# Kernel optimization log

Measured on AMD Instinct MI355X. Metric: run time of the kernel, lower is better.

## Reference

```python
import jax, jax.numpy as jnp
import numpy as np

ALPHA, BETA, GAMMA = 0.1, 0.15, 0.005
W1, W2, SHIFT = 10.0, 3.0, 0.0


def _pairwise_sq_dist(x):
    # x: [B, C, N] -> [B, N, N] of sum_c (x[..,n] - x[..,m])^2, computed cdist-style
    # to avoid materializing the [B, C, N, N] broadcasted intermediate.
    sq = jnp.sum(x * x, axis=1)                      # [B, N]
    gram = jnp.einsum('bcn,bcm->bnm', x, x)          # [B, N, N]
    d = sq[:, :, None] + sq[:, None, :] - 2.0 * gram
    return jnp.maximum(d, 0.0)


def setup_inputs() -> dict:
    key = jax.random.key(0)
    k1, k2, k3 = jax.random.split(key, 3)
    B, CG, CF, H, W, N = 8, 3, 128, 224, 224, 2048
    guidance = jax.random.normal(k1, (B, CG, H, W), dtype=jnp.float32)
    features = jax.random.normal(k2, (B, CF, H, W), dtype=jnp.float32)
    coords = jax.random.randint(k3, (2, N), 0, H)    # H == W == 224
    return {"guidance": guidance, "features": features, "coords": coords}


def reference(guidance, features, coords):
    H, W = guidance.shape[2], guidance.shape[3]
    # normalized coordinates: [2, N]
    norm_coords = coords.astype(jnp.float32) / jnp.array([[H], [W]], dtype=jnp.float32)
    # coord_diff: [1, N, N]
    coord_diff = jnp.sum(
        (norm_coords[:, :, None] - norm_coords[:, None, :]) ** 2, axis=0
    )[None]

    # gather sampled pixels: [B, C, N]
    sel_guidance = guidance[:, :, coords[0], coords[1]]
    sel_feats = features[:, :, coords[0], coords[1]]

    guidance_diff = _pairwise_sq_dist(sel_guidance)  # [B, N, N]
    feat_diff = _pairwise_sq_dist(sel_feats)         # [B, N, N]

    sim_kernel = (
        W1 * jnp.exp(-coord_diff / (2.0 * ALPHA) - guidance_diff / (2.0 * BETA))
        + W2 * jnp.exp(-coord_diff / (2.0 * GAMMA))
        - SHIFT
    )
    return jnp.mean(feat_diff * sim_kernel)
```

## Files before the change

kernel.cpp:

```cpp
#include <hip/hip_runtime.h>
#include <hip/hip_bf16.h>

#define BATCH 8
#define CGUID 3
#define CFEAT 128
#define IMH 224
#define IMW 224
#define NPTS 2048
#define HWSZ (IMH * IMW)

#define TILES 16
#define NPAIR 136
#define BM 128
#define BK 64
#define LDT 72

typedef __attribute__((ext_vector_type(8))) short bf16x8;
typedef __attribute__((ext_vector_type(4))) float f32x4;

__device__ __forceinline__ ushort f2bf(float f) {
  unsigned x = __float_as_uint(f);
  unsigned r = (x + 0x7fffu + ((x >> 16) & 1u)) >> 16;
  return (ushort)r;
}
__device__ __forceinline__ float bf2f(ushort u) {
  return __uint_as_float(((unsigned)u) << 16);
}

__global__ __launch_bounds__(256) void gather_kernel(
    const float* __restrict__ guidance, const float* __restrict__ features,
    const int* __restrict__ coords,
    ushort* __restrict__ selF, float4* __restrict__ g4, float2* __restrict__ c2)
{
  int wid  = threadIdx.x >> 6;
  int lane = threadIdx.x & 63;
  int pid  = blockIdx.x * 4 + wid;
  int b = pid >> 11;
  int n = pid & (NPTS - 1);

  int y = coords[n];
  int x = coords[NPTS + n];

  size_t fbase = ((size_t)b * CFEAT) * HWSZ + (size_t)y * IMW + x;
  float f0 = features[fbase + (size_t)lane * HWSZ];
  float f1 = features[fbase + (size_t)(lane + 64) * HWSZ];

  ushort u0 = f2bf(f0), u1 = f2bf(f1);
  size_t so = (size_t)pid * CFEAT;
  selF[so + lane]      = u0;
  selF[so + 64 + lane] = u1;

  float ff0 = bf2f(u0), ff1 = bf2f(u1);
  float s = ff0 * ff0 + ff1 * ff1;
  #pragma unroll
  for (int o = 32; o > 0; o >>= 1) s += __shfl_down(s, o);

  float gc = 0.f;
  if (lane < CGUID)
    gc = guidance[((size_t)b * CGUID + lane) * HWSZ + (size_t)y * IMW + x];
  float g0 = __shfl(gc, 0), g1 = __shfl(gc, 1), g2 = __shfl(gc, 2);

  if (lane == 0) {
    g4[pid] = make_float4(g0, g1, g2, s);
    if (b == 0)
      c2[n] = make_float2((float)y / 224.0f, (float)x / 224.0f);
  }
}

__global__ __launch_bounds__(256) void crf_kernel(
    const ushort* __restrict__ selF, const float4* __restrict__ g4,
    const float2* __restrict__ c2, float* __restrict__ out)
{
  __shared__ ushort As[BM * LDT];
  __shared__ ushort Bs[BM * LDT];
  __shared__ float4 egN[BM], egM[BM];
  __shared__ float2 ecN[BM], ecM[BM];
  __shared__ float red[4];

  int b = blockIdx.x / NPAIR;
  int p = blockIdx.x % NPAIR;
  int ti = 0, rem = p;
  while (rem >= TILES - ti) { rem -= TILES - ti; ++ti; }
  int tj = ti + rem;
  int nb0 = ti * BM, mb0 = tj * BM;

  int t = threadIdx.x;
  int lane = t & 63, wid = t >> 6;
  int wr = wid >> 1, wc = wid & 1;

  if (t < BM) {
    egN[t] = g4[b * NPTS + nb0 + t];
    ecN[t] = c2[nb0 + t];
  } else {
    int q = t - BM;
    egM[q] = g4[b * NPTS + mb0 + q];
    ecM[q] = c2[mb0 + q];
  }

  f32x4 acc[4][4];
  #pragma unroll
  for (int i = 0; i < 4; ++i)
    #pragma unroll
    for (int j = 0; j < 4; ++j) acc[i][j] = (f32x4)0.f;

  const ushort* SA = selF + ((size_t)b * NPTS + nb0) * CFEAT;
  const ushort* SB = selF + ((size_t)b * NPTS + mb0) * CFEAT;

  for (int kk = 0; kk < 2; ++kk) {
    __syncthreads();
    #pragma unroll
    for (int pass = 0; pass < 4; ++pass) {
      int idx = t + pass * 256;
      int row = idx >> 3, q = idx & 7;
      int4 va = *(const int4*)(SA + (size_t)row * CFEAT + kk * BK + q * 8);
      *(int4*)(&As[row * LDT + q * 8]) = va;
      int4 vb = *(const int4*)(SB + (size_t)row * CFEAT + kk * BK + q * 8);
      *(int4*)(&Bs[row * LDT + q * 8]) = vb;
    }
    __syncthreads();
    #pragma unroll
    for (int k2 = 0; k2 < 2; ++k2) {
      int kb = k2 * 32 + (lane >> 4) * 8;
      bf16x8 a[4], bv[4];
      #pragma unroll
      for (int i = 0; i < 4; ++i)
        a[i] = *(const bf16x8*)(&As[(wr * 64 + i * 16 + (lane & 15)) * LDT + kb]);
      #pragma unroll
      for (int j = 0; j < 4; ++j)
        bv[j] = *(const bf16x8*)(&Bs[(wc * 64 + j * 16 + (lane & 15)) * LDT + kb]);
      #pragma unroll
      for (int i = 0; i < 4; ++i)
        #pragma unroll
        for (int j = 0; j < 4; ++j)
          acc[i][j] = __builtin_amdgcn_mfma_f32_16x16x32_bf16(a[i], bv[j], acc[i][j], 0, 0, 0);
    }
  }

  float sum = 0.f;
  int mlo = lane & 15, nhi = lane >> 4;
  #pragma unroll
  for (int i = 0; i < 4; ++i) {
    #pragma unroll
    for (int r = 0; r < 4; ++r) {
      int n = wr * 64 + i * 16 + nhi * 4 + r;
      float4 gn = egN[n];
      float2 cn = ecN[n];
      #pragma unroll
      for (int j = 0; j < 4; ++j) {
        int m = wc * 64 + j * 16 + mlo;
        float4 gm = egM[m];
        float2 cm = ecM[m];
        float df = gn.w + gm.w - 2.0f * acc[i][j][r];
        df = fmaxf(df, 0.0f);
        float d0 = gn.x - gm.x, d1 = gn.y - gm.y, d2 = gn.z - gm.z;
        float dg = d0 * d0 + d1 * d1 + d2 * d2;
        float dy = cn.x - cm.x, dx = cn.y - cm.y;
        float dc = dy * dy + dx * dx;
        float sim = 10.0f * __expf(-5.0f * dc - 3.3333333f * dg)
                  +  3.0f * __expf(-100.0f * dc);
        sum += df * sim;
      }
    }
  }

  #pragma unroll
  for (int o = 32; o > 0; o >>= 1) sum += __shfl_down(sum, o);
  if (lane == 0) red[wid] = sum;
  __syncthreads();
  if (t == 0) {
    float tot = red[0] + red[1] + red[2] + red[3];
    float factor = (ti == tj ? 1.0f : 2.0f) * (1.0f / (8.0f * 2048.0f * 2048.0f));
    atomicAdd(out, tot * factor);
  }
}

extern "C" void kernel_launch(void* const* d_in, const int* in_sizes, int n_in,
                              void* d_out, int out_size, void* d_ws, size_t ws_size,
                              hipStream_t stream) {
  const float* guidance = (const float*)d_in[0];
  const float* features = (const float*)d_in[1];
  const int*   coords   = (const int*)d_in[2];
  float* out = (float*)d_out;

  char* ws = (char*)d_ws;
  ushort* selF = (ushort*)ws;
  float4* g4   = (float4*)(ws + (size_t)BATCH * NPTS * CFEAT * 2);
  float2* c2   = (float2*)(ws + (size_t)BATCH * NPTS * CFEAT * 2
                              + (size_t)BATCH * NPTS * 16);

  hipMemsetAsync(d_out, 0, sizeof(float), stream);
  gather_kernel<<<BATCH * NPTS / 4, 256, 0, stream>>>(guidance, features, coords,
                                                      selF, g4, c2);
  crf_kernel<<<BATCH * NPAIR, 256, 0, stream>>>(selF, g4, c2, out);
}
```

Before: 303.2 us.

## Sort sample points by row and gather features channel-major with transpose pass

Adds a single-block counting sort of the sample coordinates by row, so neighbouring threads gather from nearby pixels and share cache lines. The gather is restructured so each thread handles one point across 16 channels, with coalesced channel-major stores, atomic accumulation of squared norms, and a separate transpose kernel that produces the point-major bf16 layout the MFMA kernel expects. The memset is folded into the sort kernel. This adds two extra launches, a serial prefix scan in one block, and an extra round trip through the workspace.

```diff
diff --git a/kernel.cpp b/kernel.cpp
--- a/kernel.cpp
+++ b/kernel.cpp
@@ -27,54 +27,104 @@
   return __uint_as_float(((unsigned)u) << 16);
 }
 
+__global__ __launch_bounds__(256) void sort_kernel(
+    const int* __restrict__ coords,
+    int* __restrict__ slin, float2* __restrict__ sc2,
+    float* __restrict__ sq, float* __restrict__ out)
+{
+  __shared__ int ys[NPTS], xs[NPTS];
+  __shared__ int hist[IMH], offs[IMH];
+  int t = threadIdx.x;
+  for (int i = t; i < IMH; i += 256) hist[i] = 0;
+  __syncthreads();
+  for (int i = t; i < NPTS; i += 256) {
+    int y = coords[i], x = coords[NPTS + i];
+    ys[i] = y; xs[i] = x;
+    atomicAdd(&hist[y], 1);
+  }
+  __syncthreads();
+  if (t == 0) {
+    int run = 0;
+    for (int i = 0; i < IMH; ++i) { offs[i] = run; run += hist[i]; }
+  }
+  __syncthreads();
+  for (int i = t; i < NPTS; i += 256) {
+    int y = ys[i], x = xs[i];
+    int r = atomicAdd(&offs[y], 1);
+    slin[r] = y * IMW + x;
+    sc2[r] = make_float2((float)y / 224.0f, (float)x / 224.0f);
+  }
+  for (int i = t; i < BATCH * NPTS; i += 256) sq[i] = 0.0f;
+  if (t == 0) out[0] = 0.0f;
+}
+
 __global__ __launch_bounds__(256) void gather_kernel(
-    const float* __restrict__ guidance, const float* __restrict__ features,
-    const int* __restrict__ coords,
-    ushort* __restrict__ selF, float4* __restrict__ g4, float2* __restrict__ c2)
-{
-  int wid  = threadIdx.x >> 6;
-  int lane = threadIdx.x & 63;
-  int pid  = blockIdx.x * 4 + wid;
-  int b = pid >> 11;
-  int n = pid & (NPTS - 1);
-
-  int y = coords[n];
-  int x = coords[NPTS + n];
-
-  size_t fbase = ((size_t)b * CFEAT) * HWSZ + (size_t)y * IMW + x;
-  float f0 = features[fbase + (size_t)lane * HWSZ];
-  float f1 = features[fbase + (size_t)(lane + 64) * HWSZ];
-
-  ushort u0 = f2bf(f0), u1 = f2bf(f1);
-  size_t so = (size_t)pid * CFEAT;
-  selF[so + lane]      = u0;
-  selF[so + 64 + lane] = u1;
-
-  float ff0 = bf2f(u0), ff1 = bf2f(u1);
-  float s = ff0 * ff0 + ff1 * ff1;
-  #pragma unroll
-  for (int o = 32; o > 0; o >>= 1) s += __shfl_down(s, o);
-
-  float gc = 0.f;
-  if (lane < CGUID)
-    gc = guidance[((size_t)b * CGUID + lane) * HWSZ + (size_t)y * IMW + x];
-  float g0 = __shfl(gc, 0), g1 = __shfl(gc, 1), g2 = __shfl(gc, 2);
-
-  if (lane == 0) {
-    g4[pid] = make_float4(g0, g1, g2, s);
-    if (b == 0)
-      c2[n] = make_float2((float)y / 224.0f, (float)x / 224.0f);
+    const float* __restrict__ features, const float* __restrict__ guidance,
+    const int* __restrict__ slin,
+    ushort* __restrict__ selT, float4* __restrict__ gxyz, float* __restrict__ sq)
+{
+  int blk = blockIdx.x;
+  int cg = blk & 7, pg = (blk >> 3) & 7, b = blk >> 6;
+  int t = threadIdx.x;
+  int p = pg * 256 + t;
+  int lin = slin[p];
+  const float* fb = features + (size_t)b * CFEAT * HWSZ + lin;
+  float s = 0.0f;
+  #pragma unroll
+  for (int i = 0; i < 16; ++i) {
+    int c = cg * 16 + i;
+    float v = fb[(size_t)c * HWSZ];
+    ushort u = f2bf(v);
+    float fv = bf2f(u);
+    s += fv * fv;
+    selT[((size_t)(b * CFEAT + c)) * NPTS + p] = u;
+  }
+  atomicAdd(&sq[b * NPTS + p], s);
+  if (cg == 0) {
+    const float* gb = guidance + (size_t)b * CGUID * HWSZ + lin;
+    gxyz[b * NPTS + p] = make_float4(gb[0], gb[HWSZ], gb[2 * HWSZ], 0.0f);
+  }
+}
+
+__global__ __launch_bounds__(256) void transpose_kernel(
+    const ushort* __restrict__ selT, ushort* __restrict__ selF)
+{
+  __shared__ ushort Ls[CFEAT][LDT];
+  int blk = blockIdx.x;
+  int b = blk >> 5, nt = blk & 31;
+  int nb = nt * 64;
+  int t = threadIdx.x;
+  #pragma unroll
+  for (int pass = 0; pass < 4; ++pass) {
+    int idx = pass * 256 + t;
+    int c = idx >> 3, q = idx & 7;
+    int4 v = *(const int4*)(selT + ((size_t)(b * CFEAT + c)) * NPTS + nb + q * 8);
+    *(int4*)(&Ls[c][q * 8]) = v;
+  }
+  __syncthreads();
+  #pragma unroll
+  for (int pass = 0; pass < 4; ++pass) {
+    int idx = pass * 256 + t;
+    int n = idx >> 4, q = idx & 15;
+    unsigned w0 = (unsigned)Ls[q * 8 + 0][n] | ((unsigned)Ls[q * 8 + 1][n] << 16);
+    unsigned w1 = (unsigned)Ls[q * 8 + 2][n] | ((unsigned)Ls[q * 8 + 3][n] << 16);
+    unsigned w2 = (unsigned)Ls[q * 8 + 4][n] | ((unsigned)Ls[q * 8 + 5][n] << 16);
+    unsigned w3 = (unsigned)Ls[q * 8 + 6][n] | ((unsigned)Ls[q * 8 + 7][n] << 16);
+    int4 o; o.x = (int)w0; o.y = (int)w1; o.z = (int)w2; o.w = (int)w3;
+    *(int4*)(selF + ((size_t)(b * NPTS + nb + n)) * CFEAT + q * 8) = o;
   }
 }
 
 __global__ __launch_bounds__(256) void crf_kernel(
-    const ushort* __restrict__ selF, const float4* __restrict__ g4,
-    const float2* __restrict__ c2, float* __restrict__ out)
+    const ushort* __restrict__ selF, const float4* __restrict__ gxyz,
+    const float* __restrict__ sq, const float2* __restrict__ sc2,
+    float* __restrict__ out)
 {
   __shared__ ushort As[BM * LDT];
   __shared__ ushort Bs[BM * LDT];
   __shared__ float4 egN[BM], egM[BM];
   __shared__ float2 ecN[BM], ecM[BM];
+  __shared__ float sqN[BM], sqM[BM];
   __shared__ float red[4];
 
   int b = blockIdx.x / NPAIR;
@@ -89,12 +139,14 @@
   int wr = wid >> 1, wc = wid & 1;
 
   if (t < BM) {
-    egN[t] = g4[b * NPTS + nb0 + t];
-    ecN[t] = c2[nb0 + t];
+    egN[t] = gxyz[b * NPTS + nb0 + t];
+    sqN[t] = sq[b * NPTS + nb0 + t];
+    ecN[t] = sc2[nb0 + t];
   } else {
     int q = t - BM;
-    egM[q] = g4[b * NPTS + mb0 + q];
-    ecM[q] = c2[mb0 + q];
+    egM[q] = gxyz[b * NPTS + mb0 + q];
+    sqM[q] = sq[b * NPTS + mb0 + q];
+    ecM[q] = sc2[mb0 + q];
   }
 
   f32x4 acc[4][4];
@@ -145,12 +197,13 @@
       int n = wr * 64 + i * 16 + nhi * 4 + r;
       float4 gn = egN[n];
       float2 cn = ecN[n];
+      float sn = sqN[n];
       #pragma unroll
       for (int j = 0; j < 4; ++j) {
         int m = wc * 64 + j * 16 + mlo;
         float4 gm = egM[m];
         float2 cm = ecM[m];
-        float df = gn.w + gm.w - 2.0f * acc[i][j][r];
+        float df = sn + sqM[m] - 2.0f * acc[i][j][r];
         df = fmaxf(df, 0.0f);
         float d0 = gn.x - gm.x, d1 = gn.y - gm.y, d2 = gn.z - gm.z;
         float dg = d0 * d0 + d1 * d1 + d2 * d2;
@@ -183,13 +236,17 @@
   float* out = (float*)d_out;
 
   char* ws = (char*)d_ws;
-  ushort* selF = (ushort*)ws;
-  float4* g4   = (float4*)(ws + (size_t)BATCH * NPTS * CFEAT * 2);
-  float2* c2   = (float2*)(ws + (size_t)BATCH * NPTS * CFEAT * 2
-                              + (size_t)BATCH * NPTS * 16);
-
-  hipMemsetAsync(d_out, 0, sizeof(float), stream);
-  gather_kernel<<<BATCH * NPTS / 4, 256, 0, stream>>>(guidance, features, coords,
-                                                      selF, g4, c2);
-  crf_kernel<<<BATCH * NPAIR, 256, 0, stream>>>(selF, g4, c2, out);
-}
+  size_t off = 0;
+  ushort* selT = (ushort*)(ws + off); off += (size_t)BATCH * CFEAT * NPTS * 2;
+  ushort* selF = (ushort*)(ws + off); off += (size_t)BATCH * NPTS * CFEAT * 2;
+  float4* gxyz = (float4*)(ws + off); off += (size_t)BATCH * NPTS * 16;
+  float*  sqv  = (float*) (ws + off); off += (size_t)BATCH * NPTS * 4;
+  float2* sc2  = (float2*)(ws + off); off += (size_t)NPTS * 8;
+  int*    slin = (int*)   (ws + off); off += (size_t)NPTS * 4;
+
+  sort_kernel<<<1, 256, 0, stream>>>(coords, slin, sc2, sqv, out);
+  gather_kernel<<<BATCH * 8 * 8, 256, 0, stream>>>(features, guidance, slin,
+                                                   selT, gxyz, sqv);
+  transpose_kernel<<<BATCH * 32, 256, 0, stream>>>(selT, selF);
+  crf_kernel<<<BATCH * NPAIR, 256, 0, stream>>>(selF, gxyz, sqv, sc2, out);
+}
```

Result: slower. 313.1 us (+3.3%).
